# Optimization experiments

Hardware: AMD Instinct MI355X
Metric: run time of the kernel (lower is better)

Reference implementation:

```python
import jax, jax.numpy as jnp
import numpy as np

N_NODES = 50000
N_EDGES = 500000
D = 128  # in_size == out_size


def setup_inputs() -> dict:
    key = jax.random.key(0)
    ks = jax.random.split(key, 12)
    s = 1.0 / np.sqrt(D)
    feats = jax.random.normal(ks[0], (N_NODES, D), dtype=jnp.float32)
    # per-etype Linear params (torch Linear: y = x @ W.T + b)
    W_chem = jax.random.uniform(ks[1], (D, D), jnp.float32, -s, s)
    b_chem = jax.random.uniform(ks[2], (D,), jnp.float32, -s, s)
    W_elec = jax.random.uniform(ks[3], (D, D), jnp.float32, -s, s)
    b_elec = jax.random.uniform(ks[4], (D,), jnp.float32, -s, s)
    W_out = jax.random.uniform(ks[5], (D, D), jnp.float32, -s, s)
    b_out = jax.random.uniform(ks[6], (D,), jnp.float32, -s, s)
    src_chem = jax.random.randint(ks[7], (N_EDGES,), 0, N_NODES, dtype=jnp.int32)
    dst_chem = jax.random.randint(ks[8], (N_EDGES,), 0, N_NODES, dtype=jnp.int32)
    src_elec = jax.random.randint(ks[9], (N_EDGES,), 0, N_NODES, dtype=jnp.int32)
    dst_elec = jax.random.randint(ks[10], (N_EDGES,), 0, N_NODES, dtype=jnp.int32)
    return {
        "feats": feats,
        "W_chem": W_chem, "b_chem": b_chem,
        "W_elec": W_elec, "b_elec": b_elec,
        "W_out": W_out, "b_out": b_out,
        "src_chem": src_chem, "dst_chem": dst_chem,
        "src_elec": src_elec, "dst_elec": dst_elec,
    }


def reference(feats, W_chem, b_chem, W_elec, b_elec, W_out, b_out,
              src_chem, dst_chem, src_elec, dst_elec):
    n = feats.shape[0]
    # Per-etype linear projection of all node features
    Wh_chem = feats @ W_chem.T + b_chem  # [N, D]
    Wh_elec = feats @ W_elec.T + b_elec  # [N, D]
    # copy_src + sum scatter-aggregation per etype, merged with 'sum'
    h = jax.ops.segment_sum(Wh_chem[src_chem], dst_chem, num_segments=n)
    h = h + jax.ops.segment_sum(Wh_elec[src_elec], dst_elec, num_segments=n)
    # output Linear plus the last-iterated etype's Wh (quirk of original code:
    # 'electrical' is last in etypes order)
    return h @ W_out.T + b_out + Wh_elec
```

## Files before the change

### kernel.cpp

```cpp
#include <hip/hip_runtime.h>

#define D 128
#define ROW 48
#define SLOTS 46

typedef __attribute__((ext_vector_type(8))) short bf16x8;
typedef __attribute__((ext_vector_type(4))) float f32x4;

__device__ __forceinline__ unsigned short f2bf(float x) {
    unsigned int u = __float_as_uint(x);
    u += 0x7fffu + ((u >> 16) & 1u);
    return (unsigned short)(u >> 16);
}
__device__ __forceinline__ unsigned int pk2(float lo, float hi) {
    return ((unsigned int)f2bf(hi) << 16) | (unsigned int)f2bf(lo);
}
__device__ __forceinline__ float bf_lo(unsigned int u) { return __uint_as_float(u << 16); }
__device__ __forceinline__ float bf_hi(unsigned int u) { return __uint_as_float(u & 0xffff0000u); }

#define ACC8(U, P, Q)                                   \
        P.x += bf_lo(U.x); P.y += bf_hi(U.x);           \
        P.z += bf_lo(U.y); P.w += bf_hi(U.y);           \
        Q.x += bf_lo(U.z); Q.y += bf_hi(U.z);           \
        Q.z += bf_lo(U.w); Q.w += bf_hi(U.w);

__device__ __forceinline__ void agg_row(const unsigned short* __restrict__ fbf,
                                        const unsigned short* __restrict__ csr2,
                                        unsigned short* __restrict__ S,
                                        int v, int off) {
    const unsigned short* row = csr2 + (size_t)v * ROW;
    const int deg = min(*(const int*)row, SLOTS);
    float4 a0 = make_float4(0.f,0.f,0.f,0.f), b0 = make_float4(0.f,0.f,0.f,0.f);
    float4 a1 = make_float4(0.f,0.f,0.f,0.f), b1 = make_float4(0.f,0.f,0.f,0.f);
    float4 a2 = make_float4(0.f,0.f,0.f,0.f), b2 = make_float4(0.f,0.f,0.f,0.f);
    float4 a3 = make_float4(0.f,0.f,0.f,0.f), b3 = make_float4(0.f,0.f,0.f,0.f);
    int e = 0;
    for (; e + 4 <= deg; e += 4) {
        int i0 = row[2 + e + 0];
        int i1 = row[2 + e + 1];
        int i2 = row[2 + e + 2];
        int i3 = row[2 + e + 3];
        uint4 u0 = *(const uint4*)(fbf + (size_t)i0 * D + off);
        uint4 u1 = *(const uint4*)(fbf + (size_t)i1 * D + off);
        uint4 u2 = *(const uint4*)(fbf + (size_t)i2 * D + off);
        uint4 u3 = *(const uint4*)(fbf + (size_t)i3 * D + off);
        ACC8(u0, a0, b0) ACC8(u1, a1, b1) ACC8(u2, a2, b2) ACC8(u3, a3, b3)
    }
    for (; e < deg; ++e) {
        int sv = row[2 + e];
        uint4 u = *(const uint4*)(fbf + (size_t)sv * D + off);
        ACC8(u, a0, b0)
    }
    a0.x += a1.x + a2.x + a3.x;  a0.y += a1.y + a2.y + a3.y;
    a0.z += a1.z + a2.z + a3.z;  a0.w += a1.w + a2.w + a3.w;
    b0.x += b1.x + b2.x + b3.x;  b0.y += b1.y + b2.y + b3.y;
    b0.z += b1.z + b2.z + b3.z;  b0.w += b1.w + b2.w + b3.w;
    uint4 o;
    o.x = pk2(a0.x, a0.y); o.y = pk2(a0.z, a0.w);
    o.z = pk2(b0.x, b0.y); o.w = pk2(b0.z, b0.w);
    *(uint4*)(S + (size_t)v * D + off) = o;
}

__global__ __launch_bounds__(256) void wzero(
    const float* __restrict__ Wc, const float* __restrict__ We,
    const float* __restrict__ Wo, const float* __restrict__ b_c,
    const float* __restrict__ b_e, const float* __restrict__ b_o,
    unsigned short* __restrict__ wall, float* __restrict__ bco,
    float* __restrict__ beo, float* __restrict__ bsum,
    uint4* __restrict__ z4, int nz4) {
    const int id = blockIdx.x * 256 + threadIdx.x;
    const uint4 zz = make_uint4(0u, 0u, 0u, 0u);
    for (int i = id; i < nz4; i += gridDim.x * 256) z4[i] = zz;
    if (id < 16384) {
        const int j = id >> 7, k = id & 127;
        float s1 = 0.f, s2 = 0.f;
        for (int m = 0; m < 128; ++m) {
            float wo = Wo[j * 128 + m];
            s1 = fmaf(wo, Wc[m * 128 + k], s1);
            s2 = fmaf(wo, We[m * 128 + k], s2);
        }
        wall[j * 128 + k]         = f2bf(s1);
        wall[16384 + j * 128 + k] = f2bf(s2);
        wall[32768 + j * 128 + k] = f2bf(We[j * 128 + k]);
        if (k == 0) {
            float t1 = 0.f, t2 = 0.f;
            for (int m = 0; m < 128; ++m) {
                float wo = Wo[j * 128 + m];
                t1 = fmaf(wo, b_c[m], t1);
                t2 = fmaf(wo, b_e[m], t2);
            }
            bco[j] = t1; beo[j] = t2; bsum[j] = b_o[j] + b_e[j];
        }
    }
}

__global__ __launch_bounds__(256) void fillcv(
    const float4* __restrict__ f, uint4* __restrict__ o, int n8,
    const int* __restrict__ sc, const int* __restrict__ dc,
    unsigned short* __restrict__ csr2, int E) {
    int i = blockIdx.x * 256 + threadIdx.x;
    if (i < n8) {
        float4 a = f[2 * i];
        float4 b = f[2 * i + 1];
        o[i] = make_uint4(pk2(a.x, a.y), pk2(a.z, a.w), pk2(b.x, b.y), pk2(b.z, b.w));
    }
    if (i < E) {
        int d = dc[i], s = sc[i];
        unsigned short* rowp = csr2 + (size_t)d * ROW;
        int pos = atomicAdd((int*)rowp, 1);
        if (pos < SLOTS) rowp[2 + pos] = (unsigned short)s;
    }
}

__global__ __launch_bounds__(256) void fe_ac(
    const unsigned short* __restrict__ fbf,
    const int* __restrict__ se, const int* __restrict__ de,
    unsigned short* __restrict__ csr2,
    unsigned short* __restrict__ S,
    int E, int N, int nf, int total) {
    const int bid = blockIdx.x;
    const int f0 = (int)(((long long)bid * nf) / total);
    const int f1 = (int)(((long long)(bid + 1) * nf) / total);
    if (f1 > f0) {
        const int i = f0 * 256 + threadIdx.x;
        if (i < E) {
            int d = de[i] + N, s = se[i];
            unsigned short* rowp = csr2 + (size_t)d * ROW;
            int pos = atomicAdd((int*)rowp, 1);
            if (pos < SLOTS) rowp[2 + pos] = (unsigned short)s;
        }
    } else {
        const int aidx = bid - f0;
        const int wv  = threadIdx.x >> 6;
        const int ln  = threadIdx.x & 63;
        const int sub = ln >> 4;
        const int l16 = ln & 15;
        const int v = aidx * 16 + wv * 4 + sub;
        if (v < N) agg_row(fbf, csr2, S, v, l16 * 8);
    }
}

__global__ __launch_bounds__(1024) void aggregate_bf(const unsigned short* __restrict__ fbf,
                                                     const unsigned short* __restrict__ csr2,
                                                     unsigned short* __restrict__ S,
                                                     int base, int nend) {
    const int wv  = threadIdx.x >> 6;
    const int ln  = threadIdx.x & 63;
    const int sub = ln >> 4;
    const int l16 = ln & 15;
    const int v   = base + blockIdx.x * 64 + wv * 4 + sub;
    if (v < nend) agg_row(fbf, csr2, S, v, l16 * 8);
}

__global__ __launch_bounds__(512, 4) void gemm_db(
    const unsigned short* __restrict__ S,
    const unsigned short* __restrict__ fbf,
    const unsigned short* __restrict__ wall,
    const float* __restrict__ bco, const float* __restrict__ beo,
    const float* __restrict__ bsum,
    const unsigned short* __restrict__ csr2,
    float* __restrict__ out, int M) {
    __shared__ unsigned int Wt[2][8192];

    const int t    = threadIdx.x;
    const int r0   = blockIdx.x * 128;
    const int w    = t >> 6;
    const int lane = t & 63;
    const int ln   = lane & 15;
    const int quad = lane >> 4;
    const int lnx  = ln & 7;

    const int r      = r0 + w * 16 + ln;
    const bool valid = (r < M);
    const bf16x8 azero = {0, 0, 0, 0, 0, 0, 0, 0};
    const unsigned short* ap0 = S + (size_t)r * 128 + quad * 8;
    const unsigned short* ap1 = S + (size_t)(M + r) * 128 + quad * 8;
    const unsigned short* ap2 = fbf + (size_t)r * 128 + quad * 8;

    f32x4 acc[8];
#pragma unroll
    for (int g = 0; g < 8; ++g) acc[g] = (f32x4){0.f, 0.f, 0.f, 0.f};

    int soff[4], doff[4];
#pragma unroll
    for (int i2 = 0; i2 < 4; ++i2) {
        const int g2 = i2 * 512 + t;
        const int j  = g2 >> 4;
        const int cc = g2 & 15;
        soff[i2] = j * 128 + cc * 8;
        doff[i2] = j * 64 + ((cc ^ (j & 7)) << 2);
    }
    uint4 u[4];

#define LOADW(P)                                                                \
    _Pragma("unroll") for (int i2 = 0; i2 < 4; ++i2)                            \
        u[i2] = *(const uint4*)(wall + (size_t)(P) * 16384 + soff[i2]);
#define WRITEW(BUF)                                                             \
    _Pragma("unroll") for (int i2 = 0; i2 < 4; ++i2)                            \
        *(uint4*)(&Wt[BUF][doff[i2]]) = u[i2];

#define PHASE(AP, BUF)                                                               \
    {                                                                                \
        bf16x8 a[4];                                                                 \
        _Pragma("unroll") for (int ks = 0; ks < 4; ++ks)                             \
            a[ks] = valid ? *(const bf16x8*)((AP) + ks * 32) : azero;                \
        _Pragma("unroll") for (int ks = 0; ks < 4; ++ks) {                           \
            const int cx = (((ks * 4 + quad) ^ lnx) << 2);                           \
            _Pragma("unroll") for (int g = 0; g < 8; ++g) {                          \
                bf16x8 b = *(const bf16x8*)(&Wt[BUF][(g * 16 + ln) * 64 + cx]);      \
                acc[g] = __builtin_amdgcn_mfma_f32_16x16x32_bf16(a[ks], b, acc[g],   \
                                                                 0, 0, 0);           \
            }                                                                        \
        }                                                                            \
    }

    LOADW(0) WRITEW(0)
    __syncthreads();
    LOADW(1)
    PHASE(ap0, 0)
    WRITEW(1)
    __syncthreads();
    LOADW(2)
    PHASE(ap1, 1)
    WRITEW(0)
    __syncthreads();
    PHASE(ap2, 0)
#undef PHASE
#undef WRITEW
#undef LOADW

    float dcv[4], dev[4];
    int   rrv[4];
#pragma unroll
    for (int rg = 0; rg < 4; ++rg) {
        const int rr = r0 + w * 16 + quad * 4 + rg;
        rrv[rg] = rr;
        dcv[rg] = (rr < M) ? (float)(*(const int*)(csr2 + (size_t)rr * ROW)) : 0.f;
        dev[rg] = (rr < M) ? (float)(*(const int*)(csr2 + (size_t)(M + rr) * ROW)) : 0.f;
    }
#pragma unroll
    for (int g = 0; g < 8; ++g) {
        const int col = g * 16 + ln;
        const float bc = bco[col], be = beo[col], bs = bsum[col];
#pragma unroll
        for (int rg = 0; rg < 4; ++rg) {
            if (rrv[rg] < M) {
                out[(size_t)rrv[rg] * 128 + col] =
                    acc[g][rg] + bs + dcv[rg] * bc + dev[rg] * be;
            }
        }
    }
}


extern "C" void kernel_launch(void* const* d_in, const int* in_sizes, int n_in,
                              void* d_out, int out_size, void* d_ws, size_t ws_size,
                              hipStream_t stream) {
    const float* feats  = (const float*)d_in[0];
    const float* W_chem = (const float*)d_in[1];
    const float* b_chem = (const float*)d_in[2];
    const float* W_elec = (const float*)d_in[3];
    const float* b_elec = (const float*)d_in[4];
    const float* W_out  = (const float*)d_in[5];
    const float* b_out  = (const float*)d_in[6];
    const int* src_chem = (const int*)d_in[7];
    const int* dst_chem = (const int*)d_in[8];
    const int* src_elec = (const int*)d_in[9];
    const int* dst_elec = (const int*)d_in[10];
    float* out = (float*)d_out;

    const int N = in_sizes[0] / D;
    const int E = in_sizes[7];
    const int N2 = 2 * N;

    unsigned short* fbf  = (unsigned short*)d_ws;
    unsigned short* S    = fbf + (size_t)N * D;
    unsigned short* wall = S + (size_t)N2 * D;
    float* bco  = (float*)(wall + 3 * 16384);
    float* beo  = bco + 128;
    float* bsum = beo + 128;
    unsigned short* csr2 = (unsigned short*)(bsum + 128);

    const int n8 = N * D / 8;
    const int nz4 = N2 * ROW / 8;
    const int nf = (E + 255) / 256;
    const int na = (N + 15) / 16;
    const int total1 = nf + na;

    wzero<<<512, 256, 0, stream>>>(W_chem, W_elec, W_out, b_chem, b_elec, b_out,
                                   wall, bco, beo, bsum, (uint4*)csr2, nz4);
    fillcv<<<(n8 + 255) / 256, 256, 0, stream>>>(
        (const float4*)feats, (uint4*)fbf, n8, src_chem, dst_chem, csr2, E);
    fe_ac<<<total1, 256, 0, stream>>>(fbf, src_elec, dst_elec, csr2, S,
                                      E, N, nf, total1);
    aggregate_bf<<<(N + 63) / 64, 1024, 0, stream>>>(fbf, csr2, S, N, N2);
    gemm_db<<<(N + 127) / 128, 512, 0, stream>>>(S, fbf, wall, bco, beo,
                                                 bsum, csr2, out, N);
}
```

Before: 215.8 us.

## Partition second-etype aggregation into source-range passes for cache locality

The elec-edge aggregation kernel now walks each node's neighbour list several times, once per 8192-node source range. Each pass gathers only neighbours whose index falls in the current range, aiming to keep the gathered feature rows resident in cache across concurrent waves. It also uses a nontemporal store for the output row. The cost is re-reading the index list np times (about 7) and extra branching, which can cause divergence within wavefronts, and the four-way unrolled independent loads are lost.

```diff
diff --git a/kernel.cpp b/kernel.cpp
--- a/kernel.cpp
+++ b/kernel.cpp
@@ -6,6 +6,7 @@
 
 typedef __attribute__((ext_vector_type(8))) short bf16x8;
 typedef __attribute__((ext_vector_type(4))) float f32x4;
+typedef __attribute__((ext_vector_type(4))) unsigned int u32x4;
 
 __device__ __forceinline__ unsigned short f2bf(float x) {
     unsigned int u = __float_as_uint(x);
@@ -61,6 +62,31 @@
     *(uint4*)(S + (size_t)v * D + off) = o;
 }
 
+__device__ __forceinline__ void agg_row_mp(const unsigned short* __restrict__ fbf,
+                                           const unsigned short* __restrict__ csr2,
+                                           unsigned short* __restrict__ S,
+                                           int v, int off, int np) {
+    const unsigned short* row = csr2 + (size_t)v * ROW;
+    const int deg = min(*(const int*)row, SLOTS);
+    float4 a0 = make_float4(0.f,0.f,0.f,0.f), b0 = make_float4(0.f,0.f,0.f,0.f);
+    float4 a1 = make_float4(0.f,0.f,0.f,0.f), b1 = make_float4(0.f,0.f,0.f,0.f);
+    for (int pass = 0; pass < np; ++pass) {
+        for (int e = 0; e < deg; ++e) {
+            int sv = row[2 + e];
+            if ((sv >> 13) == pass) {
+                uint4 u = *(const uint4*)(fbf + (size_t)sv * D + off);
+                if (e & 1) { ACC8(u, a1, b1) } else { ACC8(u, a0, b0) }
+            }
+        }
+    }
+    a0.x += a1.x; a0.y += a1.y; a0.z += a1.z; a0.w += a1.w;
+    b0.x += b1.x; b0.y += b1.y; b0.z += b1.z; b0.w += b1.w;
+    u32x4 o;
+    o.x = pk2(a0.x, a0.y); o.y = pk2(a0.z, a0.w);
+    o.z = pk2(b0.x, b0.y); o.w = pk2(b0.z, b0.w);
+    __builtin_nontemporal_store(o, (u32x4*)(S + (size_t)v * D + off));
+}
+
 __global__ __launch_bounds__(256) void wzero(
     const float* __restrict__ Wc, const float* __restrict__ We,
     const float* __restrict__ Wo, const float* __restrict__ b_c,
@@ -140,16 +166,16 @@
     }
 }
 
-__global__ __launch_bounds__(1024) void aggregate_bf(const unsigned short* __restrict__ fbf,
+__global__ __launch_bounds__(1024) void aggregate_mp(const unsigned short* __restrict__ fbf,
                                                      const unsigned short* __restrict__ csr2,
                                                      unsigned short* __restrict__ S,
-                                                     int base, int nend) {
+                                                     int base, int nend, int np) {
     const int wv  = threadIdx.x >> 6;
     const int ln  = threadIdx.x & 63;
     const int sub = ln >> 4;
     const int l16 = ln & 15;
     const int v   = base + blockIdx.x * 64 + wv * 4 + sub;
-    if (v < nend) agg_row(fbf, csr2, S, v, l16 * 8);
+    if (v < nend) agg_row_mp(fbf, csr2, S, v, l16 * 8, np);
 }
 
 __global__ __launch_bounds__(512, 4) void gemm_db(
@@ -286,6 +312,7 @@
     const int nf = (E + 255) / 256;
     const int na = (N + 15) / 16;
     const int total1 = nf + na;
+    const int np = (N + 8191) >> 13;
 
     wzero<<<512, 256, 0, stream>>>(W_chem, W_elec, W_out, b_chem, b_elec, b_out,
                                    wall, bco, beo, bsum, (uint4*)csr2, nz4);
@@ -293,7 +320,7 @@
         (const float4*)feats, (uint4*)fbf, n8, src_chem, dst_chem, csr2, E);
     fe_ac<<<total1, 256, 0, stream>>>(fbf, src_elec, dst_elec, csr2, S,
                                       E, N, nf, total1);
-    aggregate_bf<<<(N + 63) / 64, 1024, 0, stream>>>(fbf, csr2, S, N, N2);
+    aggregate_mp<<<(N + 63) / 64, 1024, 0, stream>>>(fbf, csr2, S, N, N2, np);
     gemm_db<<<(N + 127) / 128, 512, 0, stream>>>(S, fbf, wall, bco, beo,
                                                  bsum, csr2, out, N);
 }
```

After: 295.0 us. 36.7% more time.
